# Optimization experiments

Measured on AMD Instinct MI355X. Metric: run time of the kernel, lower is better.

Reference implementation:

```python
import jax, jax.numpy as jnp
import numpy as np
from jax import lax

B, C, H, W, G = 16, 256, 96, 96, 16


def setup_inputs() -> dict:
    key = jax.random.key(0)
    ks = jax.random.split(key, 8)
    return {
        "x": jax.random.normal(ks[0], (B, C, H, W), jnp.float32),
        "in_w": jax.random.normal(ks[1], (C, C), jnp.float32) / np.sqrt(C).astype(np.float32),
        "gn1_w": jnp.ones((C,), jnp.float32),
        "gn1_b": jnp.zeros((C,), jnp.float32),
        "a_p": jnp.zeros((4, C), jnp.float32),   # torch init: zeros -> sigmoid = 0.5
        "b_p": jnp.ones((4, C), jnp.float32),
        "c_p": jnp.ones((4, C), jnp.float32),
        "d_p": jnp.ones((4, C), jnp.float32),
        "gate_w": jax.random.normal(ks[2], (C, C), jnp.float32) / np.sqrt(C).astype(np.float32),
        "gate_b": jnp.zeros((C,), jnp.float32),
        "dw_w": jax.random.normal(ks[3], (C, 1, 3, 3), jnp.float32) / 3.0,  # depthwise 3x3
        "pw_w": jax.random.normal(ks[4], (C, C), jnp.float32) / np.sqrt(C).astype(np.float32),
        "gn2_w": jnp.ones((C,), jnp.float32),
        "gn2_b": jnp.zeros((C,), jnp.float32),
    }


def group_norm(x, w, b, groups=G, eps=1e-5):
    Bn, Cn, Hn, Wn = x.shape
    xg = x.reshape(Bn, groups, Cn // groups, Hn, Wn)
    mu = xg.mean((2, 3, 4), keepdims=True)
    var = xg.var((2, 3, 4), keepdims=True)  # biased, matches torch GroupNorm
    xn = ((xg - mu) * lax.rsqrt(var + eps)).reshape(Bn, Cn, Hn, Wn)
    return xn * w[None, :, None, None] + b[None, :, None, None]


def scan_seq(seq, a, b, c, d):
    # seq: [N, C, L].  h_t = a*h_{t-1} + b*x_t ; y_t = c*h_t + d*x_t
    xs = jnp.moveaxis(seq, -1, 0)  # [L, N, C]
    def step(h, x_t):
        h = a * h + b * x_t
        return h, c * h + d * x_t
    h0 = jnp.zeros(xs.shape[1:], seq.dtype)
    _, ys = lax.scan(step, h0, xs)
    return jnp.moveaxis(ys, 0, -1)  # [N, C, L]


def scan_w(x, reverse, a, b, c, d):
    if reverse:
        x = x[:, :, :, ::-1]
    Bn, Cn, Hn, Wn = x.shape
    seq = x.transpose(0, 2, 1, 3).reshape(Bn * Hn, Cn, Wn)
    y = scan_seq(seq, a, b, c, d).reshape(Bn, Hn, Cn, Wn).transpose(0, 2, 1, 3)
    return y[:, :, :, ::-1] if reverse else y


def scan_h(x, reverse, a, b, c, d):
    if reverse:
        x = x[:, :, ::-1, :]
    Bn, Cn, Hn, Wn = x.shape
    seq = x.transpose(0, 3, 1, 2).reshape(Bn * Wn, Cn, Hn)
    y = scan_seq(seq, a, b, c, d).reshape(Bn, Wn, Cn, Hn).transpose(0, 2, 3, 1)
    return y[:, :, ::-1, :] if reverse else y


def reference(x, in_w, gn1_w, gn1_b, a_p, b_p, c_p, d_p, gate_w, gate_b, dw_w, pw_w, gn2_w, gn2_b):
    # in_proj: 1x1 conv (no bias) -> GroupNorm -> SiLU
    xp = jnp.einsum('oc,bchw->bohw', in_w, x)
    xp = jax.nn.silu(group_norm(xp, gn1_w, gn1_b))
    # 4-directional per-channel linear recurrences
    a = jax.nn.sigmoid(a_p)
    lr = scan_w(xp, False, a[0], b_p[0], c_p[0], d_p[0])
    rl = scan_w(xp, True,  a[1], b_p[1], c_p[1], d_p[1])
    tb = scan_h(xp, False, a[2], b_p[2], c_p[2], d_p[2])
    bt = scan_h(xp, True,  a[3], b_p[3], c_p[3], d_p[3])
    gate = jax.nn.sigmoid(jnp.einsum('oc,bchw->bohw', gate_w, xp) + gate_b[None, :, None, None])
    fused = 0.25 * (lr + rl + tb + bt) * gate
    # out_proj: depthwise 3x3 -> 1x1 conv -> GroupNorm -> SiLU
    dw = lax.conv_general_dilated(fused, dw_w, (1, 1), 'SAME',
                                  dimension_numbers=('NCHW', 'OIHW', 'NCHW'),
                                  feature_group_count=fused.shape[1])
    out = jnp.einsum('oc,bchw->bohw', pw_w, dw)
    return jax.nn.silu(group_norm(out, gn2_w, gn2_b))
```

## Files before the change

### kernel.cpp

```cpp
#include <hip/hip_runtime.h>
#include <hip/hip_bf16.h>

#define Bx 16
#define Cx 256
#define Hx 96
#define Wx 96
#define HWx 9216
#define NTOK 147456
#define Gx 16
#define GRPN 147456.0f

typedef unsigned short u16;
typedef unsigned int u32;
typedef __attribute__((ext_vector_type(8))) short short8;
typedef __attribute__((ext_vector_type(4))) float float4_;
typedef __attribute__((ext_vector_type(4))) unsigned short us4;
typedef __attribute__((ext_vector_type(8))) unsigned short us8;
typedef __attribute__((ext_vector_type(4))) unsigned int ui4;

__device__ __forceinline__ float b2f(u16 u){ u32 x = ((u32)u)<<16; float f; __builtin_memcpy(&f,&x,4); return f; }
__device__ __forceinline__ u16 f2b(float f){ u32 x; __builtin_memcpy(&x,&f,4); x += 0x7FFFu + ((x>>16)&1u); return (u16)(x>>16); }
__device__ __forceinline__ float sigm(float v){ return 1.0f/(1.0f+__expf(-v)); }

__global__ __launch_bounds__(256) void k_transpose(const float* __restrict__ X, u16* __restrict__ XT){
  __shared__ u16 tile[32][36];
  int blk = blockIdx.x;
  int ct  = blk & 7;
  int hwt = (blk >> 3) % 288;
  int b   = blk / 2304;
  int c0 = ct*32, hw0 = hwt*32;
  int t = threadIdx.x;
  int r  = t >> 3;
  int q4 = (t & 7) << 2;
  float4_ v = *(const float4_*)&X[((size_t)(b*Cx + c0 + r))*HWx + hw0 + q4];
  tile[r][q4+0]=f2b(v[0]); tile[r][q4+1]=f2b(v[1]); tile[r][q4+2]=f2b(v[2]); tile[r][q4+3]=f2b(v[3]);
  __syncthreads();
  us4 o = { tile[q4+0][r], tile[q4+1][r], tile[q4+2][r], tile[q4+3][r] };
  *(us4*)&XT[((size_t)(b*HWx + hw0 + r))*Cx + c0 + q4] = o;
}

#define BM 128
#define BN 64
#define LDA 40
#define LDB 264

template<int MODE>
__global__ __launch_bounds__(256) void k_gemm(const u16* __restrict__ A,
                                              const float* __restrict__ Wm,
                                              u16* __restrict__ Y,
                                              float* __restrict__ stats,
                                              const float* __restrict__ bias,
                                              u16* __restrict__ Sb)
{
  __shared__ u16 Ws[BN*LDB];
  __shared__ u16 As[BM*LDA];
  __shared__ float red[4][16][2];
  const int tid = threadIdx.x;
  int lin = blockIdx.x;
  int swz = (lin & 7) * 576 + (lin >> 3);
  const int n0 = (swz >> 2) * BM;
  const int o0 = (swz & 3) * BN;
  #pragma unroll
  for (int it=0; it<16; ++it){
    int cid = tid + it*256;
    int row = cid >> 6;
    int ko  = (cid & 63) << 2;
    float4_ w4 = *(const float4_*)&Wm[(size_t)(o0+row)*Cx + ko];
    us4 wb = { f2b(w4[0]), f2b(w4[1]), f2b(w4[2]), f2b(w4[3]) };
    *(us4*)&Ws[row*LDB + ko] = wb;
  }
  const int lane = tid & 63;
  const int wid  = tid >> 6;
  const int lm   = lane & 15;
  const int quad = lane >> 4;
  const int wn = wid & 1;
  const int wo = wid >> 1;
  float4_ acc[4][2];
  #pragma unroll
  for (int i=0;i<4;++i){ acc[i][0] = (float4_)0.0f; acc[i][1] = (float4_)0.0f; }
  for (int kk=0; kk<Cx; kk+=32){
    __syncthreads();
    #pragma unroll
    for (int it=0; it<2; ++it){
      int cid = tid + it*256;
      int r = cid >> 2;
      int ko = (cid & 3) << 3;
      *(ui4*)&As[r*LDA + ko] = *(const ui4*)&A[(size_t)(n0+r)*Cx + kk + ko];
    }
    __syncthreads();
    short8 af[4], bf[2];
    #pragma unroll
    for (int i=0;i<4;++i) af[i] = *(const short8*)&As[(wn*64 + i*16 + lm)*LDA + quad*8];
    #pragma unroll
    for (int j=0;j<2;++j) bf[j] = *(const short8*)&Ws[(wo*32 + j*16 + lm)*LDB + kk + quad*8];
    #pragma unroll
    for (int i=0;i<4;++i)
      #pragma unroll
      for (int j=0;j<2;++j)
        acc[i][j] = __builtin_amdgcn_mfma_f32_16x16x32_bf16(af[i], bf[j], acc[i][j], 0, 0, 0);
  }
  const int b = n0 / HWx;
  if (MODE == 1){
    #pragma unroll
    for (int i=0;i<4;++i){
      #pragma unroll
      for (int j=0;j<2;++j){
        int oc = o0 + wo*32 + j*16 + lm;
        float bb = bias[oc];
        #pragma unroll
        for (int r=0;r<4;++r){
          int row = n0 + wn*64 + i*16 + quad*4 + r;
          size_t idx = (size_t)row*Cx + oc;
          float g = sigm(acc[i][j][r] + bb);
          Y[idx] = f2b(0.25f * b2f(Sb[idx]) * g);
        }
      }
    }
  } else {
    float s0=0,s1=0,q0=0,q1=0;
    #pragma unroll
    for (int i=0;i<4;++i){
      #pragma unroll
      for (int j=0;j<2;++j){
        int oc = o0 + wo*32 + j*16 + lm;
        #pragma unroll
        for (int r=0;r<4;++r){
          int row = n0 + wn*64 + i*16 + quad*4 + r;
          float v = acc[i][j][r];
          Y[(size_t)row*Cx + oc] = f2b(v);
          if (j==0){ s0+=v; q0+=v*v; } else { s1+=v; q1+=v*v; }
        }
      }
    }
    s0 += __shfl_xor(s0,16); s0 += __shfl_xor(s0,32);
    q0 += __shfl_xor(q0,16); q0 += __shfl_xor(q0,32);
    s1 += __shfl_xor(s1,16); s1 += __shfl_xor(s1,32);
    q1 += __shfl_xor(q1,16); q1 += __shfl_xor(q1,32);
    if (tid < 128) ((float*)red)[tid] = 0.0f;
    __syncthreads();
    if (lane < 16){
      atomicAdd(&red[wo*2+0][lm][0], s0);
      atomicAdd(&red[wo*2+0][lm][1], q0);
      atomicAdd(&red[wo*2+1][lm][0], s1);
      atomicAdd(&red[wo*2+1][lm][1], q1);
    }
    __syncthreads();
    if (tid < 4){
      float ss=0, qq=0;
      #pragma unroll
      for (int k=0;k<16;++k){ ss += red[tid][k][0]; qq += red[tid][k][1]; }
      int g = (o0 >> 4) + tid;
      atomicAdd(&stats[(b*Gx + g)*2 + 0], ss);
      atomicAdd(&stats[(b*Gx + g)*2 + 1], qq);
    }
  }
}

__global__ void k_finalize(const float* __restrict__ st, float* __restrict__ mr){
  int i = threadIdx.x;
  float s = st[i*2+0], q = st[i*2+1];
  float mu  = s * (1.0f/GRPN);
  float var = q * (1.0f/GRPN) - mu*mu;
  mr[i*2+0] = mu;
  mr[i*2+1] = rsqrtf(var + 1e-5f);
}

__global__ __launch_bounds__(128) void k_scan_w(const u16* __restrict__ Y1, u16* __restrict__ Xp, u16* __restrict__ S,
    const float* __restrict__ ap, const float* __restrict__ bp, const float* __restrict__ cpr, const float* __restrict__ dp,
    const float* __restrict__ mr, const float* __restrict__ gwv, const float* __restrict__ gbv){
  int blk = blockIdx.x;
  int ch = blk & 1;
  int row = blk >> 1;
  int h = row % Hx, b = row / Hx;
  int t = threadIdx.x;
  int c = ch*128 + t;
  float A0 = sigm(ap[c]),      B0 = bp[c],      C0 = cpr[c],      D0 = dp[c];
  float A1 = sigm(ap[Cx+c]),   B1 = bp[Cx+c],   C1 = cpr[Cx+c],   D1 = dp[Cx+c];
  int g = c >> 4;
  float mu = mr[(b*Gx+g)*2], rs = mr[(b*Gx+g)*2+1];
  float gwc = gwv[c], gbc = gbv[c];
  const u16* base = Y1 + ((size_t)(b*Hx + h)*Wx)*Cx + c;
  u16* xpb = Xp + ((size_t)(b*Hx + h)*Wx)*Cx + c;
  u16* sb  = S  + ((size_t)(b*Hx + h)*Wx)*Cx + c;
  float hs = 0.0f;
  #pragma unroll 4
  for (int w=0; w<Wx; ++w){
    float xn = (b2f(base[(size_t)w*Cx]) - mu)*rs*gwc + gbc;
    u16 v = f2b(xn * sigm(xn));
    xpb[(size_t)w*Cx] = v;
    float xv = b2f(v);
    hs = A0*hs + B0*xv;
    sb[(size_t)w*Cx] = f2b(C0*hs + D0*xv);
  }
  asm volatile("" ::: "memory");
  hs = 0.0f;
  #pragma unroll 4
  for (int w=Wx-1; w>=0; --w){
    float xv = b2f(xpb[(size_t)w*Cx]);
    hs = A1*hs + B1*xv;
    sb[(size_t)w*Cx] = f2b(C1*hs + D1*xv + b2f(sb[(size_t)w*Cx]));
  }
}

__global__ __launch_bounds__(128) void k_scan_h(const u16* __restrict__ Xp, u16* __restrict__ S, u16* __restrict__ Av,
    const float* __restrict__ ap, const float* __restrict__ bp, const float* __restrict__ cpr, const float* __restrict__ dp){
  int blk = blockIdx.x;
  int ch = blk & 1;
  int col = blk >> 1;
  int w = col % Wx, b = col / Wx;
  int t = threadIdx.x;
  int c = ch*128 + t;
  float A2 = sigm(ap[2*Cx+c]), B2 = bp[2*Cx+c], C2 = cpr[2*Cx+c], D2 = dp[2*Cx+c];
  float A3 = sigm(ap[3*Cx+c]), B3 = bp[3*Cx+c], C3 = cpr[3*Cx+c], D3 = dp[3*Cx+c];
  const u16* base = Xp + ((size_t)(b*Hx)*Wx + w)*Cx + c;
  u16* av = Av + ((size_t)(b*Hx)*Wx + w)*Cx + c;
  u16* sb = S  + ((size_t)(b*Hx)*Wx + w)*Cx + c;
  float hs = 0.0f;
  #pragma unroll 4
  for (int h=0; h<Hx; ++h){
    float xv = b2f(base[(size_t)h*Wx*Cx]);
    hs = A2*hs + B2*xv;
    av[(size_t)h*Wx*Cx] = f2b(C2*hs + D2*xv);
  }
  asm volatile("" ::: "memory");
  hs = 0.0f;
  #pragma unroll 4
  for (int h=Hx-1; h>=0; --h){
    float xv = b2f(base[(size_t)h*Wx*Cx]);
    hs = A3*hs + B3*xv;
    size_t off = (size_t)h*Wx*Cx;
    sb[off] = f2b(C3*hs + D3*xv + b2f(av[off]) + b2f(sb[off]));
  }
}

__global__ __launch_bounds__(256) void k_dwconv(const u16* __restrict__ F, const float* __restrict__ dwW, u16* __restrict__ O){
  __shared__ float wl[2304];
  int t = threadIdx.x;
  #pragma unroll
  for (int i=0;i<9;++i) wl[t + i*256] = dwW[t + i*256];
  __syncthreads();
  int blk = blockIdx.x;
  int w16 = blk % (Wx/16);
  int h   = (blk/(Wx/16)) % Hx;
  int b   = blk / ((Wx/16)*Hx);
  int cq = (t & 63) << 2;
  int w0 = (w16 << 4) + ((t >> 6) << 2);
  float wt[36];
  #pragma unroll
  for (int j=0;j<9;++j) *(float4_*)&wt[4*j] = *(const float4_*)&wl[cq*9 + 4*j];
  float acc[4][4];
  #pragma unroll
  for (int ow=0;ow<4;++ow){ acc[ow][0]=0.0f; acc[ow][1]=0.0f; acc[ow][2]=0.0f; acc[ow][3]=0.0f; }
  const u16* Fb = F + ((size_t)(b*Hx)*Wx)*Cx + cq;
  #pragma unroll
  for (int ky=0; ky<3; ++ky){
    int hh = h + ky - 1;
    if (hh < 0 || hh >= Hx) continue;
    #pragma unroll
    for (int j=0; j<6; ++j){
      int ww = w0 + j - 1;
      if (ww < 0 || ww >= Wx) continue;
      us4 v = *(const us4*)&Fb[((size_t)hh*Wx + ww)*Cx];
      float f0=b2f(v[0]), f1=b2f(v[1]), f2=b2f(v[2]), f3=b2f(v[3]);
      #pragma unroll
      for (int ow = (j-2<0?0:j-2); ow <= (j<3?j:3); ++ow){
        int kidx = ky*3 + (j - ow);
        acc[ow][0] += f0 * wt[0*9 + kidx];
        acc[ow][1] += f1 * wt[1*9 + kidx];
        acc[ow][2] += f2 * wt[2*9 + kidx];
        acc[ow][3] += f3 * wt[3*9 + kidx];
      }
    }
  }
  #pragma unroll
  for (int ow=0; ow<4; ++ow){
    us4 o = { f2b(acc[ow][0]), f2b(acc[ow][1]), f2b(acc[ow][2]), f2b(acc[ow][3]) };
    *(us4*)&O[((size_t)((b*Hx+h)*Wx) + w0 + ow)*Cx + cq] = o;
  }
}

__global__ __launch_bounds__(256) void k_norm_tr(const u16* __restrict__ Y3, float* __restrict__ Out,
    const float* __restrict__ mr, const float* __restrict__ gw, const float* __restrict__ gb){
  __shared__ float tile[32][36];
  int blk = blockIdx.x;
  int ct  = blk & 7;
  int hwt = (blk >> 3) % 288;
  int b   = blk / 2304;
  int c0 = ct*32, hw0 = hwt*32;
  int t = threadIdx.x;
  int r  = t >> 3;
  int q4 = (t & 7) << 2;
  us4 v = *(const us4*)&Y3[((size_t)(b*HWx + hw0 + r))*Cx + c0 + q4];
  int g = (c0 + q4) >> 4;
  float mu = mr[(b*Gx+g)*2], rs = mr[(b*Gx+g)*2+1];
  #pragma unroll
  for (int i=0;i<4;++i){
    float xn = (b2f(v[i]) - mu)*rs*gw[c0+q4+i] + gb[c0+q4+i];
    tile[r][q4+i] = xn * sigm(xn);
  }
  __syncthreads();
  float4_ o = { tile[q4+0][r], tile[q4+1][r], tile[q4+2][r], tile[q4+3][r] };
  *(float4_*)&Out[((size_t)(b*Cx + c0 + r))*HWx + hw0 + q4] = o;
}

extern "C" void kernel_launch(void* const* d_in, const int* in_sizes, int n_in,
                              void* d_out, int out_size, void* d_ws, size_t ws_size,
                              hipStream_t stream){
  (void)in_sizes; (void)n_in; (void)out_size; (void)ws_size;
  const float* x    = (const float*)d_in[0];
  const float* in_w = (const float*)d_in[1];
  const float* gn1w = (const float*)d_in[2];
  const float* gn1b = (const float*)d_in[3];
  const float* ap   = (const float*)d_in[4];
  const float* bp   = (const float*)d_in[5];
  const float* cp   = (const float*)d_in[6];
  const float* dp   = (const float*)d_in[7];
  const float* gw   = (const float*)d_in[8];
  const float* gb   = (const float*)d_in[9];
  const float* dww  = (const float*)d_in[10];
  const float* pww  = (const float*)d_in[11];
  const float* gn2w = (const float*)d_in[12];
  const float* gn2b = (const float*)d_in[13];
  float* out = (float*)d_out;
  char* ws = (char*)d_ws;
  const size_t NB = (size_t)NTOK * Cx * 2;
  u16* xT = (u16*)(ws);
  u16* y1 = (u16*)(ws + NB);
  u16* xp = (u16*)(ws + 2*NB);
  u16* S  = (u16*)(ws + 3*NB);
  float* stats1 = (float*)(ws + 4*NB);
  float* stats2 = stats1 + 512;
  float* mr1    = stats1 + 1024;
  float* mr2    = stats1 + 1536;

  hipMemsetAsync(stats1, 0, 1024*sizeof(float), stream);

  k_transpose<<<36864, 256, 0, stream>>>(x, xT);
  k_gemm<0><<<4608, 256, 0, stream>>>(xT, in_w, y1, stats1, nullptr, nullptr);
  k_finalize<<<1, 256, 0, stream>>>(stats1, mr1);
  k_scan_w<<<Bx*Hx*2, 128, 0, stream>>>(y1, xp, S, ap, bp, cp, dp, mr1, gn1w, gn1b);
  k_scan_h<<<Bx*Wx*2, 128, 0, stream>>>(xp, S, xT, ap, bp, cp, dp);
  k_gemm<1><<<4608, 256, 0, stream>>>(xp, gw, S, nullptr, gb, S);
  k_dwconv<<<Bx*Hx*(Wx/16), 256, 0, stream>>>(S, dww, xT);
  k_gemm<0><<<4608, 256, 0, stream>>>(xT, pww, y1, stats2, nullptr, nullptr);
  k_finalize<<<1, 256, 0, stream>>>(stats2, mr2);
  k_norm_tr<<<36864, 256, 0, stream>>>(y1, out, mr2, gn2w, gn2b);
}
```

Baseline: 747.4 us.

## Merge horizontal and vertical scans into one launch with independent buffers

The W-direction and H-direction scans now run as two block ranges of a single kernel. The H blocks recompute the GroupNorm+SiLU activation straight from the GEMM output instead of waiting for the normalized tensor, so they no longer depend on the W scan. Each direction writes its own partial sum buffer, and the gate GEMM epilogue adds the two. This removes one launch and one serialization point and lets both scans fill the GPU together. In exchange the H scan reads y1 twice and redoes the sigmoid, and the gate epilogue makes an extra read.

```diff
diff --git a/kernel.cpp b/kernel.cpp
--- a/kernel.cpp
+++ b/kernel.cpp
@@ -50,7 +50,8 @@
                                               u16* __restrict__ Y,
                                               float* __restrict__ stats,
                                               const float* __restrict__ bias,
-                                              u16* __restrict__ Sb)
+                                              const u16* __restrict__ Sb,
+                                              const u16* __restrict__ Sb2)
 {
   __shared__ u16 Ws[BN*LDB];
   __shared__ u16 As[BM*LDA];
@@ -112,7 +113,8 @@
           int row = n0 + wn*64 + i*16 + quad*4 + r;
           size_t idx = (size_t)row*Cx + oc;
           float g = sigm(acc[i][j][r] + bb);
-          Y[idx] = f2b(0.25f * b2f(Sb[idx]) * g);
+          float s = b2f(Sb[idx]) + b2f(Sb2[idx]);
+          Y[idx] = f2b(0.25f * s * g);
         }
       }
     }
@@ -165,71 +167,74 @@
   mr[i*2+1] = rsqrtf(var + 1e-5f);
 }
 
-__global__ __launch_bounds__(128) void k_scan_w(const u16* __restrict__ Y1, u16* __restrict__ Xp, u16* __restrict__ S,
+__global__ __launch_bounds__(128) void k_scan2(const u16* __restrict__ Y1, u16* __restrict__ Xp,
+    u16* __restrict__ Sw, u16* __restrict__ Sh,
     const float* __restrict__ ap, const float* __restrict__ bp, const float* __restrict__ cpr, const float* __restrict__ dp,
     const float* __restrict__ mr, const float* __restrict__ gwv, const float* __restrict__ gbv){
   int blk = blockIdx.x;
-  int ch = blk & 1;
-  int row = blk >> 1;
-  int h = row % Hx, b = row / Hx;
   int t = threadIdx.x;
-  int c = ch*128 + t;
-  float A0 = sigm(ap[c]),      B0 = bp[c],      C0 = cpr[c],      D0 = dp[c];
-  float A1 = sigm(ap[Cx+c]),   B1 = bp[Cx+c],   C1 = cpr[Cx+c],   D1 = dp[Cx+c];
-  int g = c >> 4;
-  float mu = mr[(b*Gx+g)*2], rs = mr[(b*Gx+g)*2+1];
-  float gwc = gwv[c], gbc = gbv[c];
-  const u16* base = Y1 + ((size_t)(b*Hx + h)*Wx)*Cx + c;
-  u16* xpb = Xp + ((size_t)(b*Hx + h)*Wx)*Cx + c;
-  u16* sb  = S  + ((size_t)(b*Hx + h)*Wx)*Cx + c;
-  float hs = 0.0f;
-  #pragma unroll 4
-  for (int w=0; w<Wx; ++w){
-    float xn = (b2f(base[(size_t)w*Cx]) - mu)*rs*gwc + gbc;
-    u16 v = f2b(xn * sigm(xn));
-    xpb[(size_t)w*Cx] = v;
-    float xv = b2f(v);
-    hs = A0*hs + B0*xv;
-    sb[(size_t)w*Cx] = f2b(C0*hs + D0*xv);
-  }
-  asm volatile("" ::: "memory");
-  hs = 0.0f;
-  #pragma unroll 4
-  for (int w=Wx-1; w>=0; --w){
-    float xv = b2f(xpb[(size_t)w*Cx]);
-    hs = A1*hs + B1*xv;
-    sb[(size_t)w*Cx] = f2b(C1*hs + D1*xv + b2f(sb[(size_t)w*Cx]));
-  }
-}
-
-__global__ __launch_bounds__(128) void k_scan_h(const u16* __restrict__ Xp, u16* __restrict__ S, u16* __restrict__ Av,
-    const float* __restrict__ ap, const float* __restrict__ bp, const float* __restrict__ cpr, const float* __restrict__ dp){
-  int blk = blockIdx.x;
-  int ch = blk & 1;
-  int col = blk >> 1;
-  int w = col % Wx, b = col / Wx;
-  int t = threadIdx.x;
-  int c = ch*128 + t;
-  float A2 = sigm(ap[2*Cx+c]), B2 = bp[2*Cx+c], C2 = cpr[2*Cx+c], D2 = dp[2*Cx+c];
-  float A3 = sigm(ap[3*Cx+c]), B3 = bp[3*Cx+c], C3 = cpr[3*Cx+c], D3 = dp[3*Cx+c];
-  const u16* base = Xp + ((size_t)(b*Hx)*Wx + w)*Cx + c;
-  u16* av = Av + ((size_t)(b*Hx)*Wx + w)*Cx + c;
-  u16* sb = S  + ((size_t)(b*Hx)*Wx + w)*Cx + c;
-  float hs = 0.0f;
-  #pragma unroll 4
-  for (int h=0; h<Hx; ++h){
-    float xv = b2f(base[(size_t)h*Wx*Cx]);
-    hs = A2*hs + B2*xv;
-    av[(size_t)h*Wx*Cx] = f2b(C2*hs + D2*xv);
-  }
-  asm volatile("" ::: "memory");
-  hs = 0.0f;
-  #pragma unroll 4
-  for (int h=Hx-1; h>=0; --h){
-    float xv = b2f(base[(size_t)h*Wx*Cx]);
-    hs = A3*hs + B3*xv;
-    size_t off = (size_t)h*Wx*Cx;
-    sb[off] = f2b(C3*hs + D3*xv + b2f(av[off]) + b2f(sb[off]));
+  if (blk < 2*Bx*Hx){
+    int ch = blk & 1;
+    int row = blk >> 1;
+    int h = row % Hx, b = row / Hx;
+    int c = ch*128 + t;
+    float A0 = sigm(ap[c]),      B0 = bp[c],      C0 = cpr[c],      D0 = dp[c];
+    float A1 = sigm(ap[Cx+c]),   B1 = bp[Cx+c],   C1 = cpr[Cx+c],   D1 = dp[Cx+c];
+    int g = c >> 4;
+    float mu = mr[(b*Gx+g)*2], rs = mr[(b*Gx+g)*2+1];
+    float gwc = gwv[c], gbc = gbv[c];
+    const u16* base = Y1 + ((size_t)(b*Hx + h)*Wx)*Cx + c;
+    u16* xpb = Xp + ((size_t)(b*Hx + h)*Wx)*Cx + c;
+    u16* sb  = Sw + ((size_t)(b*Hx + h)*Wx)*Cx + c;
+    float hs = 0.0f;
+    #pragma unroll 4
+    for (int w=0; w<Wx; ++w){
+      float xn = (b2f(base[(size_t)w*Cx]) - mu)*rs*gwc + gbc;
+      u16 v = f2b(xn * sigm(xn));
+      xpb[(size_t)w*Cx] = v;
+      float xv = b2f(v);
+      hs = A0*hs + B0*xv;
+      sb[(size_t)w*Cx] = f2b(C0*hs + D0*xv);
+    }
+    asm volatile("" ::: "memory");
+    hs = 0.0f;
+    #pragma unroll 4
+    for (int w=Wx-1; w>=0; --w){
+      float xv = b2f(xpb[(size_t)w*Cx]);
+      hs = A1*hs + B1*xv;
+      sb[(size_t)w*Cx] = f2b(C1*hs + D1*xv + b2f(sb[(size_t)w*Cx]));
+    }
+  } else {
+    int col = blk - 2*Bx*Hx;
+    int ch = col & 1;
+    col >>= 1;
+    int w = col % Wx, b = col / Wx;
+    int c = ch*128 + t;
+    float A2 = sigm(ap[2*Cx+c]), B2 = bp[2*Cx+c], C2 = cpr[2*Cx+c], D2 = dp[2*Cx+c];
+    float A3 = sigm(ap[3*Cx+c]), B3 = bp[3*Cx+c], C3 = cpr[3*Cx+c], D3 = dp[3*Cx+c];
+    int g = c >> 4;
+    float mu = mr[(b*Gx+g)*2], rs = mr[(b*Gx+g)*2+1];
+    float gwc = gwv[c], gbc = gbv[c];
+    const u16* base = Y1 + ((size_t)(b*Hx)*Wx + w)*Cx + c;
+    u16* sb = Sh + ((size_t)(b*Hx)*Wx + w)*Cx + c;
+    float hs = 0.0f;
+    #pragma unroll 4
+    for (int h=0; h<Hx; ++h){
+      float xn = (b2f(base[(size_t)h*Wx*Cx]) - mu)*rs*gwc + gbc;
+      float xv = b2f(f2b(xn * sigm(xn)));
+      hs = A2*hs + B2*xv;
+      sb[(size_t)h*Wx*Cx] = f2b(C2*hs + D2*xv);
+    }
+    asm volatile("" ::: "memory");
+    hs = 0.0f;
+    #pragma unroll 4
+    for (int h=Hx-1; h>=0; --h){
+      float xn = (b2f(base[(size_t)h*Wx*Cx]) - mu)*rs*gwc + gbc;
+      float xv = b2f(f2b(xn * sigm(xn)));
+      hs = A3*hs + B3*xv;
+      size_t off = (size_t)h*Wx*Cx;
+      sb[off] = f2b(C3*hs + D3*xv + b2f(sb[off]));
+    }
   }
 }
 
@@ -336,13 +341,12 @@
   hipMemsetAsync(stats1, 0, 1024*sizeof(float), stream);
 
   k_transpose<<<36864, 256, 0, stream>>>(x, xT);
-  k_gemm<0><<<4608, 256, 0, stream>>>(xT, in_w, y1, stats1, nullptr, nullptr);
+  k_gemm<0><<<4608, 256, 0, stream>>>(xT, in_w, y1, stats1, nullptr, nullptr, nullptr);
   k_finalize<<<1, 256, 0, stream>>>(stats1, mr1);
-  k_scan_w<<<Bx*Hx*2, 128, 0, stream>>>(y1, xp, S, ap, bp, cp, dp, mr1, gn1w, gn1b);
-  k_scan_h<<<Bx*Wx*2, 128, 0, stream>>>(xp, S, xT, ap, bp, cp, dp);
-  k_gemm<1><<<4608, 256, 0, stream>>>(xp, gw, S, nullptr, gb, S);
-  k_dwconv<<<Bx*Hx*(Wx/16), 256, 0, stream>>>(S, dww, xT);
-  k_gemm<0><<<4608, 256, 0, stream>>>(xT, pww, y1, stats2, nullptr, nullptr);
+  k_scan2<<<2*Bx*Hx + 2*Bx*Wx, 128, 0, stream>>>(y1, xp, S, xT, ap, bp, cp, dp, mr1, gn1w, gn1b);
+  k_gemm<1><<<4608, 256, 0, stream>>>(xp, gw, S, nullptr, gb, S, xT);
+  k_dwconv<<<Bx*Hx*(Wx/16), 256, 0, stream>>>(S, dww, xp);
+  k_gemm<0><<<4608, 256, 0, stream>>>(xp, pww, y1, stats2, nullptr, nullptr, nullptr);
   k_finalize<<<1, 256, 0, stream>>>(stats2, mr2);
   k_norm_tr<<<36864, 256, 0, stream>>>(y1, out, mr2, gn2w, gn2b);
 }
```

Result: slower. 784.4 us (+4.9%).
